# Kernel optimization log

Hardware: AMD Instinct MI355X
Metric: run time of the kernel (lower is better)

The kernel has to match this reference:

```python
import jax, jax.numpy as jnp
import numpy as np

D_MODEL = 1024
N_HEADS = 16
D_KEY = 64
EPS = 1e-5


def setup_inputs() -> dict:
    key = jax.random.key(0)
    ks = jax.random.split(key, 12)
    d, h, dk = D_MODEL, N_HEADS, D_KEY
    s = lambda fan_in: 1.0 / np.sqrt(fan_in)
    inp = {
        "X": jax.random.normal(ks[0], (2, 2048, d), dtype=jnp.float32),
        "Wqkv": jax.random.uniform(ks[1], (d, 3 * h * dk), jnp.float32, -s(d), s(d)),
        "bqkv": jax.random.uniform(ks[2], (3 * h * dk,), jnp.float32, -s(d), s(d)),
        "Wo": jax.random.uniform(ks[3], (h * dk, d), jnp.float32, -s(h * dk), s(h * dk)),
        "bo": jax.random.uniform(ks[4], (d,), jnp.float32, -s(h * dk), s(h * dk)),
        "W1": jax.random.uniform(ks[5], (d, 4 * d), jnp.float32, -s(d), s(d)),
        "b1": jax.random.uniform(ks[6], (4 * d,), jnp.float32, -s(d), s(d)),
        "W2": jax.random.uniform(ks[7], (4 * d, d), jnp.float32, -s(4 * d), s(4 * d)),
        "b2": jax.random.uniform(ks[8], (d,), jnp.float32, -s(4 * d), s(4 * d)),
        "ln1_g": jnp.ones((d,), jnp.float32),
        "ln1_b": jnp.zeros((d,), jnp.float32),
        "ln2_g": jnp.ones((d,), jnp.float32),
        "ln2_b": jnp.zeros((d,), jnp.float32),
    }
    return inp


def _layernorm(x, g, b):
    mu = jnp.mean(x, axis=-1, keepdims=True)
    var = jnp.var(x, axis=-1, keepdims=True)
    return (x - mu) * jax.lax.rsqrt(var + EPS) * g + b


def _block(X, Wqkv, bqkv, Wo, bo, W1, b1, W2, b2, ln1_g, ln1_b, ln2_g, ln2_b):
    B, T, _ = X.shape
    h, dk = N_HEADS, D_KEY
    # --- causal multi-head self-attention on LN(X) ---
    Xn = _layernorm(X, ln1_g, ln1_b)
    qkv = (Xn @ Wqkv + bqkv).reshape(B, T, 3, h, dk)
    q, k, v = (jnp.moveaxis(qkv, 2, 0)[i].transpose(0, 2, 1, 3) for i in range(3))  # each [B,h,T,dk]
    scores = jnp.einsum("bhqd,bhkd->bhqk", q, k) / np.sqrt(dk).astype(np.float32)
    causal = jnp.tril(jnp.ones((T, T), dtype=bool))
    scores = jnp.where(causal, scores, -jnp.inf)
    attn = jax.nn.softmax(scores, axis=-1)
    ctx = jnp.einsum("bhqk,bhkd->bhqd", attn, v)  # [B,h,T,dk]
    ctx = ctx.transpose(0, 2, 1, 3).reshape(B, T, h * dk)
    atten = ctx @ Wo + bo
    X = X + atten  # dropout is identity in eval mode
    # --- FFN on LN(X) ---
    Xn2 = _layernorm(X, ln2_g, ln2_b)
    ffn = jax.nn.relu(Xn2 @ W1 + b1) @ W2 + b2
    return X + ffn


def reference(X, Wqkv, bqkv, Wo, bo, W1, b1, W2, b2, ln1_g, ln1_b, ln2_g, ln2_b):
    return _block(X, Wqkv, bqkv, Wo, bo, W1, b1, W2, b2, ln1_g, ln1_b, ln2_g, ln2_b)
```

## Files before the change

kernel.cpp:

```cpp
#include <hip/hip_runtime.h>
#include <hip/hip_bf16.h>

typedef __hip_bfloat16 bf16;
typedef __attribute__((ext_vector_type(8))) short short8;
typedef __attribute__((ext_vector_type(4))) float f32x4;

constexpr int D     = 1024;
constexpr int T     = 2048;
constexpr int BATCH = 2;
constexpr int ROWS  = BATCH * T;
constexpr int NH    = 16;
constexpr int DKEY  = 64;
constexpr int QKVN  = 3 * D;
constexpr int FFNN  = 4 * D;

static __device__ __forceinline__ float b2f(bf16 x) { return __bfloat162float(x); }
static __device__ __forceinline__ bf16  f2b(float x) { return __float2bfloat16(x); }
static __device__ __forceinline__ float fast_exp2(float x) { return __builtin_amdgcn_exp2f(x); }
static __device__ __forceinline__ unsigned short f2bu(float x) {
    return __bfloat16_as_ushort(__float2bfloat16(x));
}
static __device__ __forceinline__ float bits2f(unsigned short u) {
    unsigned int w = (unsigned int)u << 16;
    return __builtin_bit_cast(float, w);
}

static __device__ __forceinline__ void gload_lds16(const bf16* g, unsigned short* l) {
    __builtin_amdgcn_global_load_lds(
        (const __attribute__((address_space(1))) void*)g,
        (__attribute__((address_space(3))) void*)l,
        16, 0, 0);
}

__global__ __launch_bounds__(256) void transpose_cast(const float* __restrict__ in,
                                                      bf16* __restrict__ out,
                                                      int R, int C)
{
    __shared__ float tile[32][33];
    int c0 = blockIdx.x * 32, r0 = blockIdx.y * 32;
    int tx = threadIdx.x & 31, ty = threadIdx.x >> 5;
#pragma unroll
    for (int i = 0; i < 32; i += 8)
        tile[ty + i][tx] = in[(size_t)(r0 + ty + i) * C + c0 + tx];
    __syncthreads();
#pragma unroll
    for (int i = 0; i < 32; i += 8)
        out[(size_t)(c0 + ty + i) * R + r0 + tx] = f2b(tile[tx][ty + i]);
}

template <typename TIN>
__global__ __launch_bounds__(256) void ln_kernel(const TIN* __restrict__ X,
                                                 const float* __restrict__ g,
                                                 const float* __restrict__ b,
                                                 bf16* __restrict__ out)
{
    int row = blockIdx.x;
    int tid = threadIdx.x;
    int c0  = tid * 4;
    const TIN* xr = X + (size_t)row * D;
    float v[4];
    if constexpr (__is_same(TIN, float)) {
        float4 ld = *(const float4*)(xr + c0);
        v[0] = ld.x; v[1] = ld.y; v[2] = ld.z; v[3] = ld.w;
    } else {
        uint2 raw = *(const uint2*)(xr + c0);
        v[0] = bits2f((unsigned short)(raw.x & 0xffff));
        v[1] = bits2f((unsigned short)(raw.x >> 16));
        v[2] = bits2f((unsigned short)(raw.y & 0xffff));
        v[3] = bits2f((unsigned short)(raw.y >> 16));
    }

    float s1 = v[0] + v[1] + v[2] + v[3];
    float s2 = v[0]*v[0] + v[1]*v[1] + v[2]*v[2] + v[3]*v[3];
#pragma unroll
    for (int off = 32; off; off >>= 1) {
        s1 += __shfl_xor(s1, off);
        s2 += __shfl_xor(s2, off);
    }
    __shared__ float red[8];
    int lane = tid & 63, w = tid >> 6;
    if (lane == 0) { red[w] = s1; red[4 + w] = s2; }
    __syncthreads();
    s1 = red[0] + red[1] + red[2] + red[3];
    s2 = red[4] + red[5] + red[6] + red[7];

    float mu   = s1 * (1.0f / D);
    float var  = s2 * (1.0f / D) - mu * mu;
    float rstd = rsqrtf(var + 1e-5f);

    float4 gv = *(const float4*)(g + c0);
    float4 bv = *(const float4*)(b + c0);
    ushort4 pk;
    pk.x = f2bu((v[0] - mu) * rstd * gv.x + bv.x);
    pk.y = f2bu((v[1] - mu) * rstd * gv.y + bv.y);
    pk.z = f2bu((v[2] - mu) * rstd * gv.z + bv.z);
    pk.w = f2bu((v[3] - mu) * rstd * gv.w + bv.w);
    *(ushort4*)(out + (size_t)row * D + c0) = pk;
}

template <int BM, int RELU, int RES, int OUTF32, int SPLITZ>
__global__ __launch_bounds__(256) void mfma_gemm(
    const bf16* __restrict__ A, const bf16* __restrict__ Bt,
    const float* __restrict__ bias, const void* __restrict__ resid,
    void* __restrict__ out, float* __restrict__ part,
    int M, int N, int K, int Kstride)
{
    constexpr int MT = BM / 32;
    __shared__ __align__(16) unsigned short As[2][BM * 32];
    __shared__ __align__(16) unsigned short Bs[2][128 * 32];

    int gx = gridDim.x, gy = gridDim.y;
    int lid = (blockIdx.z * gy + blockIdx.y) * gx + blockIdx.x;
    int nwg = gx * gy * gridDim.z;
    int chunk = nwg >> 3;
    int swz = (lid & 7) * chunk + (lid >> 3);
    int bx = swz % gx;
    int by = (swz / gx) % gy;
    int bz = swz / (gx * gy);

    int tid  = threadIdx.x;
    int m0   = by * BM, n0 = bx * 128;
    int lane = tid & 63, wave = tid >> 6;
    int wm = (wave >> 1) * (MT * 16), wn = (wave & 1) * 64;
    int c15 = lane & 15, quad = lane >> 4;

    int koff = 0;
    if constexpr (SPLITZ) koff = bz * K;

    f32x4 acc[MT][4] = {};

    int srow = lane >> 2;
    int scol = (lane & 3) * 8;
    const bf16* abase = A  + (size_t)m0 * Kstride + koff;
    const bf16* bbase = Bt + (size_t)n0 * Kstride + koff;

    auto stage = [&](int buf, int kt) {
        int ko = kt * 32;
#pragma unroll
        for (int j = 0; j < 2; ++j) {
            int r = wave * 32 + j * 16;
            gload_lds16(bbase + (size_t)(r + srow) * Kstride + ko + scol,
                        &Bs[buf][r * 32]);
        }
        if constexpr (BM == 128) {
#pragma unroll
            for (int j = 0; j < 2; ++j) {
                int r = wave * 32 + j * 16;
                gload_lds16(abase + (size_t)(r + srow) * Kstride + ko + scol,
                            &As[buf][r * 32]);
            }
        } else {
            int r = wave * 16;
            gload_lds16(abase + (size_t)(r + srow) * Kstride + ko + scol,
                        &As[buf][r * 32]);
        }
    };

    int nk = K >> 5;
    stage(0, 0);
    __syncthreads();

    for (int kt = 0; kt < nk; ++kt) {
        int buf = kt & 1;
        if (kt + 1 < nk) stage(buf ^ 1, kt + 1);

        short8 af[MT], bfr[4];
#pragma unroll
        for (int t = 0; t < MT; ++t)
            af[t]  = *(const short8*)&As[buf][(wm + t * 16 + c15) * 32 + quad * 8];
#pragma unroll
        for (int t = 0; t < 4; ++t)
            bfr[t] = *(const short8*)&Bs[buf][(wn + t * 16 + c15) * 32 + quad * 8];
#pragma unroll
        for (int mt = 0; mt < MT; ++mt)
#pragma unroll
            for (int nt = 0; nt < 4; ++nt)
                acc[mt][nt] = __builtin_amdgcn_mfma_f32_16x16x32_bf16(
                    af[mt], bfr[nt], acc[mt][nt], 0, 0, 0);

        __syncthreads();
    }

#pragma unroll
    for (int mt = 0; mt < MT; ++mt) {
#pragma unroll
        for (int nt = 0; nt < 4; ++nt) {
            f32x4 v4 = acc[mt][nt];
            int gc = n0 + wn + nt * 16 + c15;
            float bb = bias[gc];
#pragma unroll
            for (int r = 0; r < 4; ++r) {
                int gr = m0 + wm + mt * 16 + quad * 4 + r;
                float v = v4[r] + bb;
                if constexpr (RELU) v = fmaxf(v, 0.0f);
                size_t idx = (size_t)gr * N + gc;
                if constexpr (RES == 1) v += b2f(((const bf16*)resid)[idx]);
                if constexpr (RES == 2) v += ((const float*)resid)[idx];
                if constexpr (OUTF32) ((float*)out)[idx] = v;
                else                  ((bf16*)out)[idx] = f2b(v);
            }
        }
    }
}

__global__ __launch_bounds__(512, 2) void gemm256_relu(
    const bf16* __restrict__ A, const bf16* __restrict__ Bt,
    const float* __restrict__ bias, bf16* __restrict__ out,
    int M, int N, int K)
{
    extern __shared__ unsigned short smem[];
    unsigned short* Abase = smem;
    unsigned short* Bbase = smem + 32768;

    int gx = gridDim.x;
    int lid = blockIdx.y * gx + blockIdx.x;
    int nwg = gx * gridDim.y;
    int chunk = nwg >> 3;
    int f = (lid & 7) * chunk + (lid >> 3);
    int bx = f % gx, by = f / gx;

    int tid  = threadIdx.x;
    int m0   = by * 256, n0 = bx * 256;
    int lane = tid & 63, wave = tid >> 6;
    int wm = wave >> 2;
    int wn = (wave & 3) * 64;
    int c15 = lane & 15, quad = lane >> 4;

    int rloc  = lane >> 3;
    int sslot = (lane & 7) ^ (rloc & 7);

    auto stageA = [&](int bufo, int k4, int ko) {
        int r0 = k4 * 64 + wave * 8;
        const bf16* g = A + (size_t)(m0 + r0 + rloc) * K + ko + sslot * 8;
        gload_lds16(g, Abase + bufo + r0 * 64);
    };
    auto stageB = [&](int bufo, int k4, int ko) {
        int r0 = k4 * 64 + wave * 8;
        const bf16* g = Bt + (size_t)(n0 + r0 + rloc) * K + ko + sslot * 8;
        gload_lds16(g, Bbase + bufo + r0 * 64);
    };
    auto ldf = [&](const unsigned short* base, int row, int kq) {
        int slot = kq ^ (row & 7);
        return *(const short8*)&base[row * 64 + slot * 8];
    };

    f32x4 acc[8][4] = {};

    int nt = K >> 6;
#pragma unroll
    for (int k4 = 0; k4 < 4; ++k4) stageA(0, k4, 0);
#pragma unroll
    for (int k4 = 0; k4 < 4; ++k4) stageB(0, k4, 0);

    for (int t = 0; t < nt; ++t) {
        int co = (t & 1) * 16384, no = co ^ 16384;
        bool more = (t + 1 < nt);
        int ko1 = (t + 1) * 64;
        const unsigned short* Ac = Abase + co;
        const unsigned short* Bc = Bbase + co;

        if (more) {
            stageA(no, 0, ko1);
            stageA(no, 1, ko1);
            asm volatile("s_waitcnt vmcnt(2)" ::: "memory");
        } else {
            asm volatile("s_waitcnt vmcnt(0)" ::: "memory");
        }
        __builtin_amdgcn_s_barrier();

#pragma unroll
        for (int p = 0; p < 4; ++p) {
            const int mh = p >> 1, kq0 = (p & 1) * 4 + quad;
            short8 af[4], bf[4];
#pragma unroll
            for (int i = 0; i < 4; ++i)
                af[i] = ldf(Ac, wm * 128 + mh * 64 + i * 16 + c15, kq0);
#pragma unroll
            for (int j = 0; j < 4; ++j)
                bf[j] = ldf(Bc, wn + j * 16 + c15, kq0);
            if (more) {
                if (p == 0) { stageA(no, 2, ko1); stageA(no, 3, ko1); }
                if (p == 1) { stageB(no, 0, ko1); stageB(no, 1, ko1); }
                if (p == 2) { stageB(no, 2, ko1); stageB(no, 3, ko1); }
            }
            __builtin_amdgcn_s_barrier();
            asm volatile("s_waitcnt lgkmcnt(0)" ::: "memory");
            __builtin_amdgcn_sched_barrier(0);
            __builtin_amdgcn_s_setprio(1);
#pragma unroll
            for (int i = 0; i < 4; ++i)
#pragma unroll
                for (int j = 0; j < 4; ++j)
                    acc[mh * 4 + i][j] = __builtin_amdgcn_mfma_f32_16x16x32_bf16(
                        af[i], bf[j], acc[mh * 4 + i][j], 0, 0, 0);
            __builtin_amdgcn_s_setprio(0);
            __builtin_amdgcn_s_barrier();
        }
    }

#pragma unroll
    for (int fr = 0; fr < 8; ++fr) {
#pragma unroll
        for (int j = 0; j < 4; ++j) {
            int gc = n0 + wn + j * 16 + c15;
            float bb = bias[gc];
#pragma unroll
            for (int r = 0; r < 4; ++r) {
                int gr = m0 + wm * 128 + fr * 16 + quad * 4 + r;
                float v = fmaxf(acc[fr][j][r] + bb, 0.0f);
                out[(size_t)gr * N + gc] = f2b(v);
            }
        }
    }
}

__global__ __launch_bounds__(512, 2) void gemm_w2(
    const bf16* __restrict__ A, const bf16* __restrict__ Bt,
    float* __restrict__ outP, float* __restrict__ part,
    int M, int N, int K, int Kstride)
{
    extern __shared__ unsigned short smem[];
    unsigned short* Abase = smem;
    unsigned short* Bbase = smem + 32768;

    int gx = gridDim.x, gy = gridDim.y;
    int lid = (blockIdx.z * gy + blockIdx.y) * gx + blockIdx.x;
    int nwg = gx * gy * gridDim.z;
    int chunk = nwg >> 3;
    int f = (lid & 7) * chunk + (lid >> 3);
    int bx = f % gx;
    int by = (f / gx) % gy;
    int bz = f / (gx * gy);

    int tid  = threadIdx.x;
    int m0   = by * 256, n0 = bx * 128;
    int koff = bz * K;
    int lane = tid & 63, wave = tid >> 6;
    int wm = wave >> 1;
    int wn = (wave & 1) * 64;
    int c15 = lane & 15, quad = lane >> 4;

    int rloc  = lane >> 3;
    int sslot = (lane & 7) ^ (rloc & 7);

    auto stageA = [&](int bufo, int g8, int ko) {
        int r0 = g8 * 64 + wave * 8;
        const bf16* g = A + (size_t)(m0 + r0 + rloc) * Kstride + ko + sslot * 8;
        gload_lds16(g, Abase + bufo + r0 * 64);
    };
    auto stageB = [&](int bufo, int g8, int ko) {
        int r0 = g8 * 64 + wave * 8;
        const bf16* g = Bt + (size_t)(n0 + r0 + rloc) * Kstride + ko + sslot * 8;
        gload_lds16(g, Bbase + bufo + r0 * 64);
    };
    auto ldf = [&](const unsigned short* base, int row, int kq) {
        int slot = kq ^ (row & 7);
        return *(const short8*)&base[row * 64 + slot * 8];
    };

    f32x4 acc[4][4] = {};

    int nt = K >> 6;
#pragma unroll
    for (int g8 = 0; g8 < 4; ++g8) stageA(0, g8, koff);
#pragma unroll
    for (int g8 = 0; g8 < 2; ++g8) stageB(0, g8, koff);

    for (int t = 0; t < nt; ++t) {
        int coA = (t & 1) * 16384, noA = coA ^ 16384;
        int coB = (t & 1) * 8192,  noB = coB ^ 8192;
        bool more = (t + 1 < nt);
        int ko1 = koff + (t + 1) * 64;
        const unsigned short* Ac = Abase + coA;
        const unsigned short* Bc = Bbase + coB;

        if (more) {
            stageA(noA, 0, ko1);
            stageA(noA, 1, ko1);
            asm volatile("s_waitcnt vmcnt(2)" ::: "memory");
        } else {
            asm volatile("s_waitcnt vmcnt(0)" ::: "memory");
        }
        __builtin_amdgcn_s_barrier();

#pragma unroll
        for (int p = 0; p < 2; ++p) {
            const int kq0 = p * 4 + quad;
            short8 af[4], bf[4];
#pragma unroll
            for (int i = 0; i < 4; ++i)
                af[i] = ldf(Ac, wm * 64 + i * 16 + c15, kq0);
#pragma unroll
            for (int j = 0; j < 4; ++j)
                bf[j] = ldf(Bc, wn + j * 16 + c15, kq0);
            if (more) {
                if (p == 0) { stageA(noA, 2, ko1); stageA(noA, 3, ko1); }
                if (p == 1) { stageB(noB, 0, ko1); stageB(noB, 1, ko1); }
            }
            __builtin_amdgcn_s_barrier();
            asm volatile("s_waitcnt lgkmcnt(0)" ::: "memory");
            __builtin_amdgcn_sched_barrier(0);
            __builtin_amdgcn_s_setprio(1);
#pragma unroll
            for (int i = 0; i < 4; ++i)
#pragma unroll
                for (int j = 0; j < 4; ++j)
                    acc[i][j] = __builtin_amdgcn_mfma_f32_16x16x32_bf16(
                        af[i], bf[j], acc[i][j], 0, 0, 0);
            __builtin_amdgcn_s_setprio(0);
            __builtin_amdgcn_s_barrier();
        }
    }

    float* dst = (bz == 0) ? outP : part;
#pragma unroll
    for (int i = 0; i < 4; ++i) {
#pragma unroll
        for (int j = 0; j < 4; ++j) {
            int gc = n0 + wn + j * 16 + c15;
#pragma unroll
            for (int r = 0; r < 4; ++r) {
                int gr = m0 + wm * 64 + i * 16 + quad * 4 + r;
                dst[(size_t)gr * N + gc] = acc[i][j][r];
            }
        }
    }
}

__global__ __launch_bounds__(256) void w2_reduce(float* __restrict__ out,
                                                 const float* __restrict__ part,
                                                 const float* __restrict__ bias,
                                                 const bf16* __restrict__ resid)
{
    int i = blockIdx.x * 256 + threadIdx.x;
    int col = (i & (D / 4 - 1)) * 4;
    f32x4 a = ((const f32x4*)out)[i];
    f32x4 p = ((const f32x4*)part)[i];
    float4 bb = *(const float4*)(bias + col);
    uint2 rr = ((const uint2*)resid)[i];
    a[0] += p[0] + bb.x + bits2f((unsigned short)(rr.x & 0xffff));
    a[1] += p[1] + bb.y + bits2f((unsigned short)(rr.x >> 16));
    a[2] += p[2] + bb.z + bits2f((unsigned short)(rr.y & 0xffff));
    a[3] += p[3] + bb.w + bits2f((unsigned short)(rr.y >> 16));
    ((f32x4*)out)[i] = a;
}

__global__ __launch_bounds__(256) void flash_attn(const bf16* __restrict__ qkv,
                                                  bf16* __restrict__ ctx)
{
    constexpr int KROW = 72;
    constexpr float CSC = 0.18033688011112042f;
    constexpr float MSH = 12.0f;

    __shared__ __align__(16) unsigned short Qs[64 * KROW];
    __shared__ __align__(16) unsigned short Ks[64 * KROW];
    __shared__ __align__(16) unsigned short Vt[64 * KROW];
    unsigned short* Pt = Qs;

    int bx = blockIdx.x;
    int bh = bx & 31;
    int qi = 31 - (bx >> 5);
    int h  = bh & 15, b = bh >> 4;
    int q0 = qi * 64;

    int tid = threadIdx.x, lane = tid & 63, w = tid >> 6;
    int c15 = lane & 15, quad = lane >> 4;

    const bf16* base = qkv + (size_t)b * T * QKVN;

    {
        int row = tid >> 2, qtr = tid & 3;
        const bf16* src = base + (size_t)(q0 + row) * QKVN + h * 64 + qtr * 16;
        unsigned short* dst = &Qs[row * KROW + qtr * 16];
        uint4 v0 = *(const uint4*)(src);
        uint4 v1 = *(const uint4*)(src + 8);
        *(uint4*)(dst)     = v0;
        *(uint4*)(dst + 8) = v1;
    }
    __syncthreads();

    short8 qf[2];
#pragma unroll
    for (int s = 0; s < 2; ++s)
        qf[s] = *(const short8*)&Qs[(w * 16 + c15) * KROW + s * 32 + quad * 8];

    short8 ones;
#pragma unroll
    for (int i = 0; i < 8; ++i) ones[i] = (short)0x3F80;

    f32x4 Ot[4] = {};
    f32x4 lacc  = {};

    int nkt   = q0 / 64 + 1;
    int wqmin = q0 + w * 16;

    int key = tid >> 2, seg = tid & 3;
    int keyp = (tid & 31) * 2, dk0 = (tid >> 5) * 8;

    uint4 kv0, kv1, vv0, vv1;
    {
        const bf16* ksrc = base + (size_t)key * QKVN + D + h * 64 + seg * 16;
        kv0 = *(const uint4*)ksrc;
        kv1 = *(const uint4*)(ksrc + 8);
        const bf16* vsrc = base + (size_t)keyp * QKVN + 2 * D + h * 64 + dk0;
        vv0 = *(const uint4*)vsrc;
        vv1 = *(const uint4*)(vsrc + QKVN);
    }

    for (int kt = 0; kt < nkt; ++kt) {
        int k0 = kt * 64;

        __syncthreads();
        {
            unsigned short* kd = &Ks[key * KROW + seg * 16];
            *(uint4*)kd       = kv0;
            *(uint4*)(kd + 8) = kv1;
            const unsigned short* lo = (const unsigned short*)&vv0;
            const unsigned short* hi = (const unsigned short*)&vv1;
#pragma unroll
            for (int j = 0; j < 8; ++j) {
                unsigned int pk = (unsigned int)lo[j] | ((unsigned int)hi[j] << 16);
                *(unsigned int*)&Vt[(dk0 + j) * KROW + keyp] = pk;
            }
        }
        __syncthreads();

        if (kt + 1 < nkt) {
            int k1 = k0 + 64;
            const bf16* ksrc = base + (size_t)(k1 + key) * QKVN + D + h * 64 + seg * 16;
            kv0 = *(const uint4*)ksrc;
            kv1 = *(const uint4*)(ksrc + 8);
            const bf16* vsrc = base + (size_t)(k1 + keyp) * QKVN + 2 * D + h * 64 + dk0;
            vv0 = *(const uint4*)vsrc;
            vv1 = *(const uint4*)(vsrc + QKVN);
        }

        f32x4 St[4] = {};
        __builtin_amdgcn_s_setprio(1);
#pragma unroll
        for (int s = 0; s < 2; ++s)
#pragma unroll
            for (int ktm = 0; ktm < 4; ++ktm) {
                short8 kf = *(const short8*)&Ks[(ktm * 16 + c15) * KROW + s * 32 + quad * 8];
                St[ktm] = __builtin_amdgcn_mfma_f32_16x16x32_bf16(kf, qf[s], St[ktm], 0, 0, 0);
            }
        __builtin_amdgcn_s_setprio(0);

        if (kt == nkt - 1) {
            int q_g = wqmin + c15;
#pragma unroll
            for (int ktm = 0; ktm < 4; ++ktm) {
                ushort4 pk;
#pragma unroll
                for (int r = 0; r < 4; ++r) {
                    float p = fast_exp2(fmaf(St[ktm][r], CSC, -MSH));
                    if (k0 + ktm * 16 + quad * 4 + r > q_g) p = 0.0f;
                    ((unsigned short*)&pk)[r] = f2bu(p);
                }
                *(ushort4*)&Pt[(w * 16 + c15) * KROW + ktm * 16 + quad * 4] = pk;
            }
        } else {
#pragma unroll
            for (int ktm = 0; ktm < 4; ++ktm) {
                ushort4 pk;
#pragma unroll
                for (int r = 0; r < 4; ++r)
                    ((unsigned short*)&pk)[r] = f2bu(fast_exp2(fmaf(St[ktm][r], CSC, -MSH)));
                *(ushort4*)&Pt[(w * 16 + c15) * KROW + ktm * 16 + quad * 4] = pk;
            }
        }

        __builtin_amdgcn_s_setprio(1);
#pragma unroll
        for (int s = 0; s < 2; ++s) {
            short8 pf = *(const short8*)&Pt[(w * 16 + c15) * KROW + s * 32 + quad * 8];
            lacc = __builtin_amdgcn_mfma_f32_16x16x32_bf16(ones, pf, lacc, 0, 0, 0);
#pragma unroll
            for (int dt = 0; dt < 4; ++dt) {
                short8 vf = *(const short8*)&Vt[(dt * 16 + c15) * KROW + s * 32 + quad * 8];
                Ot[dt] = __builtin_amdgcn_mfma_f32_16x16x32_bf16(vf, pf, Ot[dt], 0, 0, 0);
            }
        }
        __builtin_amdgcn_s_setprio(0);
    }

    {
        float inv = 1.0f / lacc[0];
        int grow = b * T + q0 + w * 16 + c15;
        bf16* dst = ctx + (size_t)grow * D + h * 64 + quad * 4;
#pragma unroll
        for (int dt = 0; dt < 4; ++dt) {
            ushort4 pk;
#pragma unroll
            for (int r = 0; r < 4; ++r)
                ((unsigned short*)&pk)[r] = f2bu(Ot[dt][r] * inv);
            *(ushort4*)(dst + dt * 16) = pk;
        }
    }
}

extern "C" void kernel_launch(void* const* d_in, const int* in_sizes, int n_in,
                              void* d_out, int out_size, void* d_ws, size_t ws_size,
                              hipStream_t stream)
{
    const float* X    = (const float*)d_in[0];
    const float* Wqkv = (const float*)d_in[1];
    const float* bqkv = (const float*)d_in[2];
    const float* Wo   = (const float*)d_in[3];
    const float* bo   = (const float*)d_in[4];
    const float* W1   = (const float*)d_in[5];
    const float* b1   = (const float*)d_in[6];
    const float* W2   = (const float*)d_in[7];
    const float* b2   = (const float*)d_in[8];
    const float* ln1g = (const float*)d_in[9];
    const float* ln1b = (const float*)d_in[10];
    const float* ln2g = (const float*)d_in[11];
    const float* ln2b = (const float*)d_in[12];
    float* out = (float*)d_out;

    char* ws = (char*)d_ws;
    bf16* Wqkv_t = (bf16*)(ws + 0);
    bf16* Wo_t   = (bf16*)(ws + 6291456);
    bf16* W1_t   = (bf16*)(ws + 8388608);
    bf16* W2_t   = (bf16*)(ws + 16777216);
    bf16* Xn     = (bf16*)(ws + 25165824);
    bf16* X1     = Xn;
    bf16* qkv    = (bf16*)(ws + 33554432);
    bf16* Xn2    = (bf16*)(ws + 33554432);
    bf16* ctx    = (bf16*)(ws + 58720256);
    bf16* mid    = (bf16*)(ws + 41943040);
    float* W2part = (float*)(ws + 0);

    transpose_cast<<<dim3(QKVN / 32, D / 32), 256, 0, stream>>>(Wqkv, Wqkv_t, D, QKVN);
    transpose_cast<<<dim3(D / 32, D / 32), 256, 0, stream>>>(Wo, Wo_t, D, D);
    transpose_cast<<<dim3(FFNN / 32, D / 32), 256, 0, stream>>>(W1, W1_t, D, FFNN);
    transpose_cast<<<dim3(D / 32, FFNN / 32), 256, 0, stream>>>(W2, W2_t, FFNN, D);

    ln_kernel<float><<<ROWS, 256, 0, stream>>>(X, ln1g, ln1b, Xn);
    mfma_gemm<128, 0, 0, 0, 0><<<dim3(QKVN / 128, ROWS / 128), 256, 0, stream>>>(
        Xn, Wqkv_t, bqkv, nullptr, qkv, nullptr, ROWS, QKVN, D, D);
    flash_attn<<<1024, 256, 0, stream>>>(qkv, ctx);
    mfma_gemm<64, 0, 2, 0, 0><<<dim3(D / 128, ROWS / 64), 256, 0, stream>>>(
        ctx, Wo_t, bo, X, X1, nullptr, ROWS, D, D, D);
    ln_kernel<bf16><<<ROWS, 256, 0, stream>>>(X1, ln2g, ln2b, Xn2);
    gemm256_relu<<<dim3(FFNN / 256, ROWS / 256), 512, 131072, stream>>>(
        Xn2, W1_t, b1, mid, ROWS, FFNN, D);
    gemm_w2<<<dim3(D / 128, ROWS / 256, 2), 512, 98304, stream>>>(
        mid, W2_t, out, W2part, ROWS, D, FFNN / 2, FFNN);
    w2_reduce<<<ROWS * D / 4 / 256, 256, 0, stream>>>(out, W2part, b2, X1);
}
```

Measured before the change: 322.6 us.

## Pair causal query tiles per attention block and reuse 256-tile GEMM for QKV

Flash attention now runs 512-thread blocks, each handling two query tiles (i and 31-i) that share the K/V tiles loaded into shared memory. This balances the causal workload across blocks and halves redundant K/V staging. The QKV projection switches from the 128-tile mfma_gemm to the templated 256x256 gemm256 kernel with ReLU disabled. The risk is that the lighter tile in each pair sits idle at barriers while the heavier one finishes, and the QKV launch has only 192 workgroups.

```diff
diff --git a/kernel.cpp b/kernel.cpp
--- a/kernel.cpp
+++ b/kernel.cpp
@@ -203,7 +203,8 @@
     }
 }
 
-__global__ __launch_bounds__(512, 2) void gemm256_relu(
+template <int RELU>
+__global__ __launch_bounds__(512, 2) void gemm256(
     const bf16* __restrict__ A, const bf16* __restrict__ Bt,
     const float* __restrict__ bias, bf16* __restrict__ out,
     int M, int N, int K)
@@ -307,7 +308,8 @@
 #pragma unroll
             for (int r = 0; r < 4; ++r) {
                 int gr = m0 + wm * 128 + fr * 16 + quad * 4 + r;
-                float v = fmaxf(acc[fr][j][r] + bb, 0.0f);
+                float v = acc[fr][j][r] + bb;
+                if constexpr (RELU) v = fmaxf(v, 0.0f);
                 out[(size_t)gr * N + gc] = f2b(v);
             }
         }
@@ -445,32 +447,37 @@
     ((f32x4*)out)[i] = a;
 }
 
-__global__ __launch_bounds__(256) void flash_attn(const bf16* __restrict__ qkv,
+__global__ __launch_bounds__(512) void flash_attn(const bf16* __restrict__ qkv,
                                                   bf16* __restrict__ ctx)
 {
     constexpr int KROW = 72;
     constexpr float CSC = 0.18033688011112042f;
     constexpr float MSH = 12.0f;
 
-    __shared__ __align__(16) unsigned short Qs[64 * KROW];
+    __shared__ __align__(16) unsigned short Qs[128 * KROW];
     __shared__ __align__(16) unsigned short Ks[64 * KROW];
     __shared__ __align__(16) unsigned short Vt[64 * KROW];
     unsigned short* Pt = Qs;
 
     int bx = blockIdx.x;
     int bh = bx & 31;
-    int qi = 31 - (bx >> 5);
+    int pi = bx >> 5;
     int h  = bh & 15, b = bh >> 4;
-    int q0 = qi * 64;
+    int qa = pi, qb = 31 - pi;
+    int q0a = qa * 64, q0b = qb * 64;
+    int nkta = qa + 1, nktb = qb + 1;
 
     int tid = threadIdx.x, lane = tid & 63, w = tid >> 6;
+    int wq = w & 3;
+    int tb = w >> 2;
     int c15 = lane & 15, quad = lane >> 4;
 
     const bf16* base = qkv + (size_t)b * T * QKVN;
 
     {
         int row = tid >> 2, qtr = tid & 3;
-        const bf16* src = base + (size_t)(q0 + row) * QKVN + h * 64 + qtr * 16;
+        int grow = (row < 64) ? (q0a + row) : (q0b + row - 64);
+        const bf16* src = base + (size_t)grow * QKVN + h * 64 + qtr * 16;
         unsigned short* dst = &Qs[row * KROW + qtr * 16];
         uint4 v0 = *(const uint4*)(src);
         uint4 v1 = *(const uint4*)(src + 8);
@@ -479,10 +486,11 @@
     }
     __syncthreads();
 
+    int qrow_l = tb * 64 + wq * 16 + c15;
     short8 qf[2];
 #pragma unroll
     for (int s = 0; s < 2; ++s)
-        qf[s] = *(const short8*)&Qs[(w * 16 + c15) * KROW + s * 32 + quad * 8];
+        qf[s] = *(const short8*)&Qs[qrow_l * KROW + s * 32 + quad * 8];
 
     short8 ones;
 #pragma unroll
@@ -491,102 +499,102 @@
     f32x4 Ot[4] = {};
     f32x4 lacc  = {};
 
-    int nkt   = q0 / 64 + 1;
-    int wqmin = q0 + w * 16;
-
-    int key = tid >> 2, seg = tid & 3;
-    int keyp = (tid & 31) * 2, dk0 = (tid >> 5) * 8;
-
-    uint4 kv0, kv1, vv0, vv1;
+    int q0m   = tb ? q0b : q0a;
+    int nktm  = tb ? nktb : nkta;
+    int wqmin = q0m + wq * 16;
+
+    int key = tid >> 3, seg = tid & 7;
+    int keyp = (tid & 31) * 2, dkv = (tid >> 5) * 4;
+
+    uint4 kv0;
+    uint2 vv0, vv1;
     {
-        const bf16* ksrc = base + (size_t)key * QKVN + D + h * 64 + seg * 16;
+        const bf16* ksrc = base + (size_t)key * QKVN + D + h * 64 + seg * 8;
         kv0 = *(const uint4*)ksrc;
-        kv1 = *(const uint4*)(ksrc + 8);
-        const bf16* vsrc = base + (size_t)keyp * QKVN + 2 * D + h * 64 + dk0;
-        vv0 = *(const uint4*)vsrc;
-        vv1 = *(const uint4*)(vsrc + QKVN);
-    }
-
-    for (int kt = 0; kt < nkt; ++kt) {
+        const bf16* vsrc = base + (size_t)keyp * QKVN + 2 * D + h * 64 + dkv;
+        vv0 = *(const uint2*)vsrc;
+        vv1 = *(const uint2*)(vsrc + QKVN);
+    }
+
+    for (int kt = 0; kt < nktb; ++kt) {
         int k0 = kt * 64;
 
         __syncthreads();
         {
-            unsigned short* kd = &Ks[key * KROW + seg * 16];
-            *(uint4*)kd       = kv0;
-            *(uint4*)(kd + 8) = kv1;
+            *(uint4*)&Ks[key * KROW + seg * 8] = kv0;
             const unsigned short* lo = (const unsigned short*)&vv0;
             const unsigned short* hi = (const unsigned short*)&vv1;
 #pragma unroll
-            for (int j = 0; j < 8; ++j) {
+            for (int j = 0; j < 4; ++j) {
                 unsigned int pk = (unsigned int)lo[j] | ((unsigned int)hi[j] << 16);
-                *(unsigned int*)&Vt[(dk0 + j) * KROW + keyp] = pk;
+                *(unsigned int*)&Vt[(dkv + j) * KROW + keyp] = pk;
             }
         }
         __syncthreads();
 
-        if (kt + 1 < nkt) {
+        if (kt + 1 < nktb) {
             int k1 = k0 + 64;
-            const bf16* ksrc = base + (size_t)(k1 + key) * QKVN + D + h * 64 + seg * 16;
+            const bf16* ksrc = base + (size_t)(k1 + key) * QKVN + D + h * 64 + seg * 8;
             kv0 = *(const uint4*)ksrc;
-            kv1 = *(const uint4*)(ksrc + 8);
-            const bf16* vsrc = base + (size_t)(k1 + keyp) * QKVN + 2 * D + h * 64 + dk0;
-            vv0 = *(const uint4*)vsrc;
-            vv1 = *(const uint4*)(vsrc + QKVN);
-        }
-
-        f32x4 St[4] = {};
-        __builtin_amdgcn_s_setprio(1);
-#pragma unroll
-        for (int s = 0; s < 2; ++s)
-#pragma unroll
-            for (int ktm = 0; ktm < 4; ++ktm) {
-                short8 kf = *(const short8*)&Ks[(ktm * 16 + c15) * KROW + s * 32 + quad * 8];
-                St[ktm] = __builtin_amdgcn_mfma_f32_16x16x32_bf16(kf, qf[s], St[ktm], 0, 0, 0);
-            }
-        __builtin_amdgcn_s_setprio(0);
-
-        if (kt == nkt - 1) {
-            int q_g = wqmin + c15;
-#pragma unroll
-            for (int ktm = 0; ktm < 4; ++ktm) {
-                ushort4 pk;
-#pragma unroll
-                for (int r = 0; r < 4; ++r) {
-                    float p = fast_exp2(fmaf(St[ktm][r], CSC, -MSH));
-                    if (k0 + ktm * 16 + quad * 4 + r > q_g) p = 0.0f;
-                    ((unsigned short*)&pk)[r] = f2bu(p);
+            const bf16* vsrc = base + (size_t)(k1 + keyp) * QKVN + 2 * D + h * 64 + dkv;
+            vv0 = *(const uint2*)vsrc;
+            vv1 = *(const uint2*)(vsrc + QKVN);
+        }
+
+        if (kt < nktm) {
+            f32x4 St[4] = {};
+            __builtin_amdgcn_s_setprio(1);
+#pragma unroll
+            for (int s = 0; s < 2; ++s)
+#pragma unroll
+                for (int ktm = 0; ktm < 4; ++ktm) {
+                    short8 kf = *(const short8*)&Ks[(ktm * 16 + c15) * KROW + s * 32 + quad * 8];
+                    St[ktm] = __builtin_amdgcn_mfma_f32_16x16x32_bf16(kf, qf[s], St[ktm], 0, 0, 0);
                 }
-                *(ushort4*)&Pt[(w * 16 + c15) * KROW + ktm * 16 + quad * 4] = pk;
-            }
-        } else {
-#pragma unroll
-            for (int ktm = 0; ktm < 4; ++ktm) {
-                ushort4 pk;
-#pragma unroll
-                for (int r = 0; r < 4; ++r)
-                    ((unsigned short*)&pk)[r] = f2bu(fast_exp2(fmaf(St[ktm][r], CSC, -MSH)));
-                *(ushort4*)&Pt[(w * 16 + c15) * KROW + ktm * 16 + quad * 4] = pk;
-            }
-        }
-
-        __builtin_amdgcn_s_setprio(1);
-#pragma unroll
-        for (int s = 0; s < 2; ++s) {
-            short8 pf = *(const short8*)&Pt[(w * 16 + c15) * KROW + s * 32 + quad * 8];
-            lacc = __builtin_amdgcn_mfma_f32_16x16x32_bf16(ones, pf, lacc, 0, 0, 0);
-#pragma unroll
-            for (int dt = 0; dt < 4; ++dt) {
-                short8 vf = *(const short8*)&Vt[(dt * 16 + c15) * KROW + s * 32 + quad * 8];
-                Ot[dt] = __builtin_amdgcn_mfma_f32_16x16x32_bf16(vf, pf, Ot[dt], 0, 0, 0);
-            }
-        }
-        __builtin_amdgcn_s_setprio(0);
+            __builtin_amdgcn_s_setprio(0);
+
+            if (kt == nktm - 1) {
+                int q_g = wqmin + c15;
+#pragma unroll
+                for (int ktm = 0; ktm < 4; ++ktm) {
+                    ushort4 pk;
+#pragma unroll
+                    for (int r = 0; r < 4; ++r) {
+                        float p = fast_exp2(fmaf(St[ktm][r], CSC, -MSH));
+                        if (k0 + ktm * 16 + quad * 4 + r > q_g) p = 0.0f;
+                        ((unsigned short*)&pk)[r] = f2bu(p);
+                    }
+                    *(ushort4*)&Pt[qrow_l * KROW + ktm * 16 + quad * 4] = pk;
+                }
+            } else {
+#pragma unroll
+                for (int ktm = 0; ktm < 4; ++ktm) {
+                    ushort4 pk;
+#pragma unroll
+                    for (int r = 0; r < 4; ++r)
+                        ((unsigned short*)&pk)[r] = f2bu(fast_exp2(fmaf(St[ktm][r], CSC, -MSH)));
+                    *(ushort4*)&Pt[qrow_l * KROW + ktm * 16 + quad * 4] = pk;
+                }
+            }
+
+            __builtin_amdgcn_s_setprio(1);
+#pragma unroll
+            for (int s = 0; s < 2; ++s) {
+                short8 pf = *(const short8*)&Pt[qrow_l * KROW + s * 32 + quad * 8];
+                lacc = __builtin_amdgcn_mfma_f32_16x16x32_bf16(ones, pf, lacc, 0, 0, 0);
+#pragma unroll
+                for (int dt = 0; dt < 4; ++dt) {
+                    short8 vf = *(const short8*)&Vt[(dt * 16 + c15) * KROW + s * 32 + quad * 8];
+                    Ot[dt] = __builtin_amdgcn_mfma_f32_16x16x32_bf16(vf, pf, Ot[dt], 0, 0, 0);
+                }
+            }
+            __builtin_amdgcn_s_setprio(0);
+        }
     }
 
     {
         float inv = 1.0f / lacc[0];
-        int grow = b * T + q0 + w * 16 + c15;
+        int grow = b * T + q0m + wq * 16 + c15;
         bf16* dst = ctx + (size_t)grow * D + h * 64 + quad * 4;
 #pragma unroll
         for (int dt = 0; dt < 4; ++dt) {
@@ -637,13 +645,13 @@
     transpose_cast<<<dim3(D / 32, FFNN / 32), 256, 0, stream>>>(W2, W2_t, FFNN, D);
 
     ln_kernel<float><<<ROWS, 256, 0, stream>>>(X, ln1g, ln1b, Xn);
-    mfma_gemm<128, 0, 0, 0, 0><<<dim3(QKVN / 128, ROWS / 128), 256, 0, stream>>>(
-        Xn, Wqkv_t, bqkv, nullptr, qkv, nullptr, ROWS, QKVN, D, D);
-    flash_attn<<<1024, 256, 0, stream>>>(qkv, ctx);
+    gemm256<0><<<dim3(QKVN / 256, ROWS / 256), 512, 131072, stream>>>(
+        Xn, Wqkv_t, bqkv, qkv, ROWS, QKVN, D);
+    flash_attn<<<512, 512, 0, stream>>>(qkv, ctx);
     mfma_gemm<64, 0, 2, 0, 0><<<dim3(D / 128, ROWS / 64), 256, 0, stream>>>(
         ctx, Wo_t, bo, X, X1, nullptr, ROWS, D, D, D);
     ln_kernel<bf16><<<ROWS, 256, 0, stream>>>(X1, ln2g, ln2b, Xn2);
-    gemm256_relu<<<dim3(FFNN / 256, ROWS / 256), 512, 131072, stream>>>(
+    gemm256<1><<<dim3(FFNN / 256, ROWS / 256), 512, 131072, stream>>>(
         Xn2, W1_t, b1, mid, ROWS, FFNN, D);
     gemm_w2<<<dim3(D / 128, ROWS / 256, 2), 512, 98304, stream>>>(
         mid, W2_t, out, W2part, ROWS, D, FFNN / 2, FFNN);
```

After: 328.4 us. About the same (+1.8%).
